# Kernel tuning notes

Measured on AMD Instinct MI355X. Metric: run time of the kernel, lower is better.

Reference implementation:

```python
import jax, jax.numpy as jnp
import numpy as np
from jax import lax

B, N, D, K = 32, 16384, 64, 64


def setup_inputs() -> dict:
    key = jax.random.key(0)
    k1, k2 = jax.random.split(key)
    data = jax.random.normal(k1, (B, N, D), dtype=jnp.float32)
    first_idx = jax.random.randint(k2, (B,), 0, N)
    return {"data": data, "first_idx": first_idx}


def reference(data, first_idx):
    # KMeans++ init: first center chosen by given index; each subsequent center
    # is the point farthest (in euclidean distance) from its nearest chosen center.
    # torch.cdist -> min -> argmax is monotone in squared distance, so we track
    # squared distances and maintain a running min incrementally (same argmax).
    b_range = jnp.arange(B)
    first = data[b_range, first_idx]                       # (B, D)
    # squared distance of every point to the first center
    min_d = jnp.sum((data - first[:, None, :]) ** 2, axis=-1)  # (B, N)

    def step(min_d, _):
        idx = jnp.argmax(min_d, axis=1)                    # (B,) farthest point
        new_c = data[b_range, idx]                         # (B, D)
        d = jnp.sum((data - new_c[:, None, :]) ** 2, axis=-1)
        return jnp.minimum(min_d, d), new_c

    _, rest = lax.scan(step, min_d, None, length=K - 1)    # (K-1, B, D)
    centers = jnp.concatenate([first[:, None, :], jnp.moveaxis(rest, 0, 1)], axis=1)
    return centers                                         # (B, K, D)
```

## Files before the change

kernel.cpp:

```cpp
#include <hip/hip_runtime.h>


#define B_   32
#define N_   16384
#define D_   64
#define K_   64
#define T_   256
#define WPB  4
#define SLOTS_PER_K (B_ * 32)

typedef unsigned long long u64;

__device__ __forceinline__ void amax_comb(float& v, int& i, float v2, int i2) {
    if (v2 > v || (v2 == v && i2 < i)) { v = v2; i = i2; }
}

__global__ void kmpp_zero_slots(u64* __restrict__ slots, int n) {
    int i = blockIdx.x * blockDim.x + threadIdx.x;
    if (i < n) slots[i] = 0ULL;
}


template <int GSHIFT>
__global__ __launch_bounds__(T_, 4) void kmpp_coop(
    const float* __restrict__ data, const int* __restrict__ first_idx,
    u64* __restrict__ slots, float* __restrict__ centers)
{
    constexpr int gpb   = 1 << GSHIFT;
    constexpr int chunk = N_ >> GSHIFT;
    constexpr int npass = chunk / 16;
    constexpr int ppw   = chunk / 4;

    const int b    = blockIdx.x >> GSHIFT;
    const int g    = blockIdx.x & (gpb - 1);
    const int wave = threadIdx.x >> 6;
    const int lane = threadIdx.x & 63;
    const int sub  = lane >> 4;
    const int d4   = lane & 15;

    const float* __restrict__ bdata = data + (size_t)b * N_ * D_;
    const float4* __restrict__ rowp = (const float4*)bdata;
    const int lbase = wave * ppw;
    const int gbase = g * chunk;

    __shared__ float  md[chunk];
    __shared__ float4 csh[D_ / 4];
    __shared__ float  red_v[WPB];
    __shared__ int    red_i[WPB];
    __shared__ int    s_ci;

    for (int i = threadIdx.x; i < chunk; i += T_) md[i] = 3.4e38f;

    for (int k = 0; k < K_; ++k) {
        if (k == 0) {
            if (threadIdx.x == 0) s_ci = first_idx[b];
        } else if (wave == 0) {
            u64 pk = 0;
            if (lane < gpb) {
                const u64* slot = slots + (size_t)(k - 1) * SLOTS_PER_K
                                        + b * 32 + lane;
                do {
                    pk = __hip_atomic_load(slot, __ATOMIC_RELAXED,
                                           __HIP_MEMORY_SCOPE_AGENT);
                } while (pk == 0ULL);
            }
            #pragma unroll
            for (int m = 1; m < 64; m <<= 1) {
                u64 o = __shfl_xor(pk, m, 64);
                if (o > pk) pk = o;
            }
            if (lane == 0) s_ci = (int)(~(unsigned)pk) & (N_ - 1);
        }
        __syncthreads();
        const int ci = s_ci;

        if (threadIdx.x < D_ / 4)
            csh[threadIdx.x] = ((const float4*)(bdata + (size_t)ci * D_))[threadIdx.x];
        __syncthreads();
        if (g == 0 && threadIdx.x < D_ / 4)
            ((float4*)(centers + ((size_t)b * K_ + k) * D_))[threadIdx.x] = csh[threadIdx.x];
        if (k == K_ - 1) break;

        const float4 c = csh[d4];
        float bv = -1.f; int bi = 0x7fffffff;
        float4 xb[4];
        #pragma unroll
        for (int t = 0; t < 4 && t < npass; ++t)
            xb[t] = rowp[(size_t)(gbase + lbase + t * 4 + sub) * 16 + d4];
        #pragma unroll 4
        for (int t = 0; t < npass; ++t) {
            float4 x = xb[t & 3];
            if (t + 4 < npass)
                xb[t & 3] = rowp[(size_t)(gbase + lbase + (t + 4) * 4 + sub) * 16 + d4];
            float dx = x.x - c.x, dy = x.y - c.y, dz = x.z - c.z, dw = x.w - c.w;
            float s = fmaf(dx, dx, fmaf(dy, dy, fmaf(dz, dz, dw * dw)));
            s += __shfl_xor(s, 1, 64);
            s += __shfl_xor(s, 2, 64);
            s += __shfl_xor(s, 4, 64);
            s += __shfl_xor(s, 8, 64);
            const int lp = lbase + t * 4 + sub;
            float nv = fminf(md[lp], s);
            if (d4 == 0) md[lp] = nv;
            amax_comb(bv, bi, nv, gbase + lp);
        }
        #pragma unroll
        for (int m = 1; m < 64; m <<= 1) {
            float v2 = __shfl_xor(bv, m, 64);
            int   i2 = __shfl_xor(bi, m, 64);
            amax_comb(bv, bi, v2, i2);
        }
        if (lane == 0) { red_v[wave] = bv; red_i[wave] = bi; }
        __syncthreads();
        if (threadIdx.x == 0) {
            #pragma unroll
            for (int w = 1; w < WPB; ++w) amax_comb(bv, bi, red_v[w], red_i[w]);
            u64 pk = ((u64)__float_as_uint(bv) << 32) | (unsigned)(~bi);
            __hip_atomic_store(slots + (size_t)k * SLOTS_PER_K + b * 32 + g,
                               pk, __ATOMIC_RELAXED, __HIP_MEMORY_SCOPE_AGENT);
        }
    }
}


#define FG   16
#define FPPT 4
#define FCHUNK (N_ / FG)

__device__ __forceinline__ void fb_block_argmax_store(
    float v, int i, int b, int g, int parity,
    float* __restrict__ pval, int* __restrict__ pidx,
    float* red_v, int* red_i)
{
    #pragma unroll
    for (int off = 32; off > 0; off >>= 1) {
        float v2 = __shfl_down(v, off, 64);
        int   i2 = __shfl_down(i, off, 64);
        amax_comb(v, i, v2, i2);
    }
    int lane = threadIdx.x & 63;
    int wave = threadIdx.x >> 6;
    if (lane == 0) { red_v[wave] = v; red_i[wave] = i; }
    __syncthreads();
    if (threadIdx.x == 0) {
        #pragma unroll
        for (int w = 1; w < T_ / 64; ++w) amax_comb(v, i, red_v[w], red_i[w]);
        pval[(b * 2 + parity) * FG + g] = v;
        pidx[(b * 2 + parity) * FG + g] = i;
    }
}

__device__ __forceinline__ float fb_dist2(const float4* __restrict__ row,
                                          const float4* csh)
{
    float ax = 0.f, ay = 0.f, az = 0.f, aw = 0.f;
    #pragma unroll
    for (int j = 0; j < D_ / 4; ++j) {
        float4 x = row[j];
        float4 c = csh[j];
        float dx = x.x - c.x, dy = x.y - c.y, dz = x.z - c.z, dw = x.w - c.w;
        ax = fmaf(dx, dx, ax);
        ay = fmaf(dy, dy, ay);
        az = fmaf(dz, dz, az);
        aw = fmaf(dw, dw, aw);
    }
    return (ax + ay) + (az + aw);
}

__global__ __launch_bounds__(T_) void kmpp_init(
    const float* __restrict__ data, const int* __restrict__ first_idx,
    float* __restrict__ min_d, float* __restrict__ pval, int* __restrict__ pidx,
    float* __restrict__ centers)
{
    const int blk = blockIdx.x;
    const int b = blk / FG, g = blk % FG;
    __shared__ float4 csh[D_ / 4];
    __shared__ float red_v[T_ / 64];
    __shared__ int   red_i[T_ / 64];

    const int ci = first_idx[b];
    const float4* crow = (const float4*)(data + ((size_t)b * N_ + ci) * D_);
    if (threadIdx.x < D_ / 4) csh[threadIdx.x] = crow[threadIdx.x];
    __syncthreads();
    if (g == 0 && threadIdx.x < D_ / 4)
        ((float4*)(centers + (size_t)b * K_ * D_))[threadIdx.x] = csh[threadIdx.x];

    float best_v = -1.f; int best_i = 0;
    for (int m = 0; m < FPPT; ++m) {
        const int p = g * FCHUNK + m * T_ + threadIdx.x;
        const float4* row = (const float4*)(data + ((size_t)b * N_ + p) * D_);
        float d = fb_dist2(row, csh);
        min_d[(size_t)b * N_ + p] = d;
        amax_comb(best_v, best_i, d, p);
    }
    fb_block_argmax_store(best_v, best_i, b, g, 0, pval, pidx, red_v, red_i);
}

__global__ __launch_bounds__(T_) void kmpp_step(
    const float* __restrict__ data, float* __restrict__ min_d,
    float* __restrict__ pval, int* __restrict__ pidx,
    float* __restrict__ centers, int k)
{
    const int blk = blockIdx.x;
    const int b = blk / FG, g = blk % FG;
    const int pin = (k - 1) & 1, pout = k & 1;
    __shared__ float4 csh[D_ / 4];
    __shared__ float red_v[T_ / 64];
    __shared__ int   red_i[T_ / 64];
    __shared__ int   sidx;

    if (threadIdx.x == 0) {
        float v = pval[(b * 2 + pin) * FG];
        int   i = pidx[(b * 2 + pin) * FG];
        for (int gg = 1; gg < FG; ++gg)
            amax_comb(v, i, pval[(b * 2 + pin) * FG + gg], pidx[(b * 2 + pin) * FG + gg]);
        sidx = i;
    }
    __syncthreads();
    const int ci = sidx;
    const float4* crow = (const float4*)(data + ((size_t)b * N_ + ci) * D_);
    if (threadIdx.x < D_ / 4) csh[threadIdx.x] = crow[threadIdx.x];
    __syncthreads();
    if (g == 0 && threadIdx.x < D_ / 4)
        ((float4*)(centers + ((size_t)b * K_ + k) * D_))[threadIdx.x] = csh[threadIdx.x];

    if (k == K_ - 1) return;

    float best_v = -1.f; int best_i = 0;
    for (int m = 0; m < FPPT; ++m) {
        const int p = g * FCHUNK + m * T_ + threadIdx.x;
        const float4* row = (const float4*)(data + ((size_t)b * N_ + p) * D_);
        float d = fb_dist2(row, csh);
        const size_t off = (size_t)b * N_ + p;
        float nv = fminf(min_d[off], d);
        min_d[off] = nv;
        amax_comb(best_v, best_i, nv, p);
    }
    fb_block_argmax_store(best_v, best_i, b, g, pout, pval, pidx, red_v, red_i);
}


extern "C" void kernel_launch(void* const* d_in, const int* in_sizes, int n_in,
                              void* d_out, int out_size, void* d_ws, size_t ws_size,
                              hipStream_t stream)
{
    const float* data      = (const float*)d_in[0];
    const int*   first_idx = (const int*)d_in[1];
    float*       centers   = (float*)d_out;

    u64*   slots = (u64*)d_ws;
    float* min_d = (float*)d_ws;
    float* pval  = min_d + (size_t)B_ * N_;
    int*   pidx  = (int*)(pval + B_ * 2 * FG);

    int occ5 = 0, occ4 = 0;
    (void)hipOccupancyMaxActiveBlocksPerMultiprocessor(&occ5, kmpp_coop<5>, T_, 0);
    (void)hipOccupancyMaxActiveBlocksPerMultiprocessor(&occ4, kmpp_coop<4>, T_, 0);

    const void* kfn = nullptr;
    int gshift = 0;
    if (occ5 >= 4)      { kfn = (const void*)kmpp_coop<5>; gshift = 5; }
    else if (occ4 >= 2) { kfn = (const void*)kmpp_coop<4>; gshift = 4; }

    if (kfn) {
        const int nslots = K_ * SLOTS_PER_K;
        hipLaunchKernelGGL(kmpp_zero_slots, dim3((nslots + T_ - 1) / T_), dim3(T_),
                           0, stream, slots, nslots);
        void* args[] = { (void*)&data, (void*)&first_idx,
                         (void*)&slots, (void*)&centers };
        hipError_t err = hipLaunchCooperativeKernel(
            kfn, dim3(B_ << gshift), dim3(T_), args, 0, stream);
        if (err == hipSuccess) return;
        (void)hipGetLastError();
    }

    dim3 grid(B_ * FG), block(T_);
    hipLaunchKernelGGL(kmpp_init, grid, block, 0, stream,
                       data, first_idx, min_d, pval, pidx, centers);
    for (int k = 1; k < K_; ++k) {
        hipLaunchKernelGGL(kmpp_step, grid, block, 0, stream,
                           data, min_d, pval, pidx, centers, k);
    }
}
```

Measured before the change: 1.493 ms.

## Keep running min distances in registers and add a 64-block-per-batch cooperative variant

The per-point running minimum distance array moves from LDS into a fully unrolled per-thread register array, which removes the shared-memory read/write in the inner loop. A new GSHIFT=6 configuration (2048 blocks, 8 waves per EU) is tried first, and the prefetch depth becomes a template parameter (4 or 8). The spin-wait on cross-block slots now sleeps between polls, and the slot stride is widened to 64. Register pressure rises with the unrolled md array, and the higher block count depends on the occupancy check succeeding; otherwise it falls back to the older configurations.

```diff
diff --git a/kernel.cpp b/kernel.cpp
--- a/kernel.cpp
+++ b/kernel.cpp
@@ -7,7 +7,8 @@
 #define K_   64
 #define T_   256
 #define WPB  4
-#define SLOTS_PER_K (B_ * 32)
+#define GMAX 64
+#define SLOTS_PER_K (B_ * GMAX)
 
 typedef unsigned long long u64;
 
@@ -21,8 +22,8 @@
 }
 
 
-template <int GSHIFT>
-__global__ __launch_bounds__(T_, 4) void kmpp_coop(
+template <int GSHIFT, int WPEU, int DEPTH>
+__global__ __launch_bounds__(T_, WPEU) void kmpp_coop(
     const float* __restrict__ data, const int* __restrict__ first_idx,
     u64* __restrict__ slots, float* __restrict__ centers)
 {
@@ -42,14 +43,14 @@
     const float4* __restrict__ rowp = (const float4*)bdata;
     const int lbase = wave * ppw;
     const int gbase = g * chunk;
-
-    __shared__ float  md[chunk];
+    float md[npass];
+    #pragma unroll
+    for (int t = 0; t < npass; ++t) md[t] = 3.4e38f;
+
     __shared__ float4 csh[D_ / 4];
     __shared__ float  red_v[WPB];
     __shared__ int    red_i[WPB];
     __shared__ int    s_ci;
-
-    for (int i = threadIdx.x; i < chunk; i += T_) md[i] = 3.4e38f;
 
     for (int k = 0; k < K_; ++k) {
         if (k == 0) {
@@ -58,18 +59,21 @@
             u64 pk = 0;
             if (lane < gpb) {
                 const u64* slot = slots + (size_t)(k - 1) * SLOTS_PER_K
-                                        + b * 32 + lane;
-                do {
+                                        + b * GMAX + lane;
+                pk = __hip_atomic_load(slot, __ATOMIC_RELAXED,
+                                       __HIP_MEMORY_SCOPE_AGENT);
+                while (pk == 0ULL) {
+                    __builtin_amdgcn_s_sleep(2);
                     pk = __hip_atomic_load(slot, __ATOMIC_RELAXED,
                                            __HIP_MEMORY_SCOPE_AGENT);
-                } while (pk == 0ULL);
+                }
             }
             #pragma unroll
             for (int m = 1; m < 64; m <<= 1) {
                 u64 o = __shfl_xor(pk, m, 64);
                 if (o > pk) pk = o;
             }
-            if (lane == 0) s_ci = (int)(~(unsigned)pk) & (N_ - 1);
+            if (lane == 0) s_ci = (int)(~(unsigned)pk);
         }
         __syncthreads();
         const int ci = s_ci;
@@ -83,25 +87,25 @@
 
         const float4 c = csh[d4];
         float bv = -1.f; int bi = 0x7fffffff;
-        float4 xb[4];
-        #pragma unroll
-        for (int t = 0; t < 4 && t < npass; ++t)
+        float4 xb[DEPTH];
+        #pragma unroll
+        for (int t = 0; t < DEPTH && t < npass; ++t)
             xb[t] = rowp[(size_t)(gbase + lbase + t * 4 + sub) * 16 + d4];
-        #pragma unroll 4
+        #pragma unroll
         for (int t = 0; t < npass; ++t) {
-            float4 x = xb[t & 3];
-            if (t + 4 < npass)
-                xb[t & 3] = rowp[(size_t)(gbase + lbase + (t + 4) * 4 + sub) * 16 + d4];
+            float4 x = xb[t % DEPTH];
+            if (t + DEPTH < npass)
+                xb[t % DEPTH] =
+                    rowp[(size_t)(gbase + lbase + (t + DEPTH) * 4 + sub) * 16 + d4];
             float dx = x.x - c.x, dy = x.y - c.y, dz = x.z - c.z, dw = x.w - c.w;
             float s = fmaf(dx, dx, fmaf(dy, dy, fmaf(dz, dz, dw * dw)));
             s += __shfl_xor(s, 1, 64);
             s += __shfl_xor(s, 2, 64);
             s += __shfl_xor(s, 4, 64);
             s += __shfl_xor(s, 8, 64);
-            const int lp = lbase + t * 4 + sub;
-            float nv = fminf(md[lp], s);
-            if (d4 == 0) md[lp] = nv;
-            amax_comb(bv, bi, nv, gbase + lp);
+            float nv = fminf(md[t], s);
+            md[t] = nv;
+            amax_comb(bv, bi, nv, gbase + lbase + t * 4 + sub);
         }
         #pragma unroll
         for (int m = 1; m < 64; m <<= 1) {
@@ -115,7 +119,7 @@
             #pragma unroll
             for (int w = 1; w < WPB; ++w) amax_comb(bv, bi, red_v[w], red_i[w]);
             u64 pk = ((u64)__float_as_uint(bv) << 32) | (unsigned)(~bi);
-            __hip_atomic_store(slots + (size_t)k * SLOTS_PER_K + b * 32 + g,
+            __hip_atomic_store(slots + (size_t)k * SLOTS_PER_K + b * GMAX + g,
                                pk, __ATOMIC_RELAXED, __HIP_MEMORY_SCOPE_AGENT);
         }
     }
@@ -252,14 +256,16 @@
     float* pval  = min_d + (size_t)B_ * N_;
     int*   pidx  = (int*)(pval + B_ * 2 * FG);
 
-    int occ5 = 0, occ4 = 0;
-    (void)hipOccupancyMaxActiveBlocksPerMultiprocessor(&occ5, kmpp_coop<5>, T_, 0);
-    (void)hipOccupancyMaxActiveBlocksPerMultiprocessor(&occ4, kmpp_coop<4>, T_, 0);
+    int occ6 = 0, occ5 = 0, occ4 = 0;
+    (void)hipOccupancyMaxActiveBlocksPerMultiprocessor(&occ6, kmpp_coop<6, 8, 4>, T_, 0);
+    (void)hipOccupancyMaxActiveBlocksPerMultiprocessor(&occ5, kmpp_coop<5, 4, 8>, T_, 0);
+    (void)hipOccupancyMaxActiveBlocksPerMultiprocessor(&occ4, kmpp_coop<4, 4, 8>, T_, 0);
 
     const void* kfn = nullptr;
     int gshift = 0;
-    if (occ5 >= 4)      { kfn = (const void*)kmpp_coop<5>; gshift = 5; }
-    else if (occ4 >= 2) { kfn = (const void*)kmpp_coop<4>; gshift = 4; }
+    if (occ6 >= 8)      { kfn = (const void*)kmpp_coop<6, 8, 4>; gshift = 6; }
+    else if (occ5 >= 4) { kfn = (const void*)kmpp_coop<5, 4, 8>; gshift = 5; }
+    else if (occ4 >= 2) { kfn = (const void*)kmpp_coop<4, 4, 8>; gshift = 4; }
 
     if (kfn) {
         const int nslots = K_ * SLOTS_PER_K;
```

After: 3.381 ms. 127% more time.

## Pin leading rows of each block's chunk in LDS and prefetch before barrier

Applied to the files above, without the earlier changes.

Each block now copies the first PINPASS passes of every wave's rows into shared memory once and reads them from LDS on every center step, so only the rest of the chunk is streamed from global memory. The first global prefetch for the streamed part is issued at the top of the iteration, before the spin-wait and barrier, so it overlaps the inter-block synchronisation. Slot stride is widened to a GMAX constant and the index mask is dropped. Extra LDS use (32KB for GSHIFT=5) may lower occupancy and can make the launcher fall back to the smaller grid or the non-cooperative path.

```diff
diff --git a/kernel.cpp b/kernel.cpp
--- a/kernel.cpp
+++ b/kernel.cpp
@@ -7,7 +7,8 @@
 #define K_   64
 #define T_   256
 #define WPB  4
-#define SLOTS_PER_K (B_ * 32)
+#define GMAX 64
+#define SLOTS_PER_K (B_ * GMAX)
 
 typedef unsigned long long u64;
 
@@ -21,7 +22,7 @@
 }
 
 
-template <int GSHIFT>
+template <int GSHIFT, int PINPASS>
 __global__ __launch_bounds__(T_, 4) void kmpp_coop(
     const float* __restrict__ data, const int* __restrict__ first_idx,
     u64* __restrict__ slots, float* __restrict__ centers)
@@ -30,6 +31,8 @@
     constexpr int chunk = N_ >> GSHIFT;
     constexpr int npass = chunk / 16;
     constexpr int ppw   = chunk / 4;
+    constexpr int npin4 = WPB * PINPASS * 4 * 16;
+    static_assert(PINPASS % 4 == 0 && PINPASS + 4 <= npass, "pipeline bounds");
 
     const int b    = blockIdx.x >> GSHIFT;
     const int g    = blockIdx.x & (gpb - 1);
@@ -44,6 +47,7 @@
     const int gbase = g * chunk;
 
     __shared__ float  md[chunk];
+    __shared__ float4 pinned[npin4];
     __shared__ float4 csh[D_ / 4];
     __shared__ float  red_v[WPB];
     __shared__ int    red_i[WPB];
@@ -51,14 +55,28 @@
 
     for (int i = threadIdx.x; i < chunk; i += T_) md[i] = 3.4e38f;
 
+    for (int l = threadIdx.x; l < npin4; l += T_) {
+        const int dd = l & 15;
+        const int s  = l >> 4;
+        const int w  = s / (PINPASS * 4);
+        const int r  = s - w * (PINPASS * 4);
+        const int lp = w * ppw + (r >> 2) * 4 + (r & 3);
+        pinned[l] = rowp[(size_t)(gbase + lp) * 16 + dd];
+    }
+
     for (int k = 0; k < K_; ++k) {
+        float4 xb[4];
+        #pragma unroll
+        for (int j = 0; j < 4; ++j)
+            xb[j] = rowp[(size_t)(gbase + lbase + (PINPASS + j) * 4 + sub) * 16 + d4];
+
         if (k == 0) {
             if (threadIdx.x == 0) s_ci = first_idx[b];
         } else if (wave == 0) {
             u64 pk = 0;
             if (lane < gpb) {
                 const u64* slot = slots + (size_t)(k - 1) * SLOTS_PER_K
-                                        + b * 32 + lane;
+                                        + b * GMAX + lane;
                 do {
                     pk = __hip_atomic_load(slot, __ATOMIC_RELAXED,
                                            __HIP_MEMORY_SCOPE_AGENT);
@@ -69,7 +87,7 @@
                 u64 o = __shfl_xor(pk, m, 64);
                 if (o > pk) pk = o;
             }
-            if (lane == 0) s_ci = (int)(~(unsigned)pk) & (N_ - 1);
+            if (lane == 0) s_ci = (int)(~(unsigned)pk);
         }
         __syncthreads();
         const int ci = s_ci;
@@ -83,12 +101,24 @@
 
         const float4 c = csh[d4];
         float bv = -1.f; int bi = 0x7fffffff;
-        float4 xb[4];
+
         #pragma unroll
-        for (int t = 0; t < 4 && t < npass; ++t)
-            xb[t] = rowp[(size_t)(gbase + lbase + t * 4 + sub) * 16 + d4];
+        for (int t = 0; t < PINPASS; ++t) {
+            float4 x = pinned[((wave * PINPASS + t) * 4 + sub) * 16 + d4];
+            float dx = x.x - c.x, dy = x.y - c.y, dz = x.z - c.z, dw = x.w - c.w;
+            float s = fmaf(dx, dx, fmaf(dy, dy, fmaf(dz, dz, dw * dw)));
+            s += __shfl_xor(s, 1, 64);
+            s += __shfl_xor(s, 2, 64);
+            s += __shfl_xor(s, 4, 64);
+            s += __shfl_xor(s, 8, 64);
+            const int lp = lbase + t * 4 + sub;
+            float nv = fminf(md[lp], s);
+            if (d4 == 0) md[lp] = nv;
+            amax_comb(bv, bi, nv, gbase + lp);
+        }
+
         #pragma unroll 4
-        for (int t = 0; t < npass; ++t) {
+        for (int t = PINPASS; t < npass; ++t) {
             float4 x = xb[t & 3];
             if (t + 4 < npass)
                 xb[t & 3] = rowp[(size_t)(gbase + lbase + (t + 4) * 4 + sub) * 16 + d4];
@@ -103,6 +133,7 @@
             if (d4 == 0) md[lp] = nv;
             amax_comb(bv, bi, nv, gbase + lp);
         }
+
         #pragma unroll
         for (int m = 1; m < 64; m <<= 1) {
             float v2 = __shfl_xor(bv, m, 64);
@@ -115,7 +146,7 @@
             #pragma unroll
             for (int w = 1; w < WPB; ++w) amax_comb(bv, bi, red_v[w], red_i[w]);
             u64 pk = ((u64)__float_as_uint(bv) << 32) | (unsigned)(~bi);
-            __hip_atomic_store(slots + (size_t)k * SLOTS_PER_K + b * 32 + g,
+            __hip_atomic_store(slots + (size_t)k * SLOTS_PER_K + b * GMAX + g,
                                pk, __ATOMIC_RELAXED, __HIP_MEMORY_SCOPE_AGENT);
         }
     }
@@ -253,13 +284,13 @@
     int*   pidx  = (int*)(pval + B_ * 2 * FG);
 
     int occ5 = 0, occ4 = 0;
-    (void)hipOccupancyMaxActiveBlocksPerMultiprocessor(&occ5, kmpp_coop<5>, T_, 0);
-    (void)hipOccupancyMaxActiveBlocksPerMultiprocessor(&occ4, kmpp_coop<4>, T_, 0);
+    (void)hipOccupancyMaxActiveBlocksPerMultiprocessor(&occ5, kmpp_coop<5, 8>, T_, 0);
+    (void)hipOccupancyMaxActiveBlocksPerMultiprocessor(&occ4, kmpp_coop<4, 8>, T_, 0);
 
     const void* kfn = nullptr;
     int gshift = 0;
-    if (occ5 >= 4)      { kfn = (const void*)kmpp_coop<5>; gshift = 5; }
-    else if (occ4 >= 2) { kfn = (const void*)kmpp_coop<4>; gshift = 4; }
+    if (occ5 >= 4)      { kfn = (const void*)kmpp_coop<5, 8>; gshift = 5; }
+    else if (occ4 >= 2) { kfn = (const void*)kmpp_coop<4, 8>; gshift = 4; }
 
     if (kfn) {
         const int nslots = K_ * SLOTS_PER_K;
```

After: 1.435 ms. 3.9% less time.
